# Optimization experiments

Measured on AMD Instinct MI355X. Metric: run time of the kernel, lower is better.

## Reference

```python
import jax, jax.numpy as jnp
import numpy as np
from jax import lax

K = 8  # number of KNN neighbors (excluding self)


def setup_inputs() -> dict:
    key = jax.random.key(0)
    k1, k2, k3 = jax.random.split(key, 3)
    B, H, W, C = 32, 14, 14, 2048
    OUT = 512
    x = jax.random.normal(k1, (B, H, W, C), dtype=jnp.float32)
    W1 = jax.random.normal(k2, (C, OUT), dtype=jnp.float32) * (1.0 / np.sqrt(C))
    b1 = jnp.zeros((OUT,), dtype=jnp.float32)
    W2 = jax.random.normal(k3, (OUT, OUT), dtype=jnp.float32) * (1.0 / np.sqrt(OUT))
    b2 = jnp.zeros((OUT,), dtype=jnp.float32)
    return {"x": x, "W1": W1, "b1": b1, "W2": W2, "b2": b2}


def _knn_edges(xf, k):
    # full pairwise squared-euclidean distance (monotone in cdist p=2)
    sq = jnp.sum(xf * xf, axis=-1)                      # [N]
    d2 = sq[:, None] + sq[None, :] - 2.0 * (xf @ xf.T)  # [N, N]
    _, idx = lax.top_k(-d2, k + 1)                      # smallest k+1
    knn = idx[:, 1:]                                    # drop self
    N = xf.shape[0]
    src = jnp.repeat(jnp.arange(N), k)
    dst = knn.reshape(-1)
    # GCNConv adds self-loops
    loops = jnp.arange(N)
    src = jnp.concatenate([src, loops])
    dst = jnp.concatenate([dst, loops])
    return src, dst


def _gcn_conv(h, W, b, src, dst, N):
    # PyG GCNConv: sym-normalized aggregation with self-loops
    deg = jax.ops.segment_sum(jnp.ones_like(dst, dtype=h.dtype), dst, num_segments=N)
    dinv = lax.rsqrt(jnp.maximum(deg, 1.0))
    norm = dinv[src] * dinv[dst]                        # [E]
    hw = h @ W                                          # [N, F]
    msg = hw[src] * norm[:, None]                       # gather + scale
    out = jax.ops.segment_sum(msg, dst, num_segments=N) # scatter-add
    return out + b


def reference(x, W1, b1, W2, b2):
    B, H, Wd, C = x.shape
    N = B * H * Wd
    xf = x.reshape(N, C)
    src, dst = _knn_edges(xf, K)
    h = jax.nn.relu(_gcn_conv(xf, W1, b1, src, dst, N))
    # dropout is identity in eval mode
    h = jax.nn.relu(_gcn_conv(h, W2, b2, src, dst, N))
    return h.reshape(B, H, Wd, W2.shape[1])
```

## Files before the change

kernel.cpp:

```cpp
#include <hip/hip_runtime.h>

typedef __attribute__((ext_vector_type(8))) _Float16 half8;
typedef __attribute__((ext_vector_type(4))) _Float16 half4;
typedef __attribute__((ext_vector_type(4))) float f32x4;

#define N_NODES 6272
#define CDIM    2048
#define ODIM    512
#define NPAN    49
#define NSLOT   392
#define GRID_G  1232
#define GATE    0.6f

#define XHI_OFF    0ul
#define CANDV_OFF  25690112ul
#define CANDI_OFF  35524608ul
#define SQ_OFF     40441856ul
#define KNN_OFF    40466944ul
#define C16_OFF    40667648ul
#define V16_OFF    41069056ul
#define DEG_OFF    41470464ul
#define CNT_OFF    41495552ul
#define DINV_OFF   41520640ul
#define RPTR_OFF   41545728ul
#define COL_OFF    41571072ul
#define W1T_OFF    41796864ul
#define W2T_OFF    43894016ul
#define HW_OFF     CANDV_OFF
#define H1H_OFF    44418304ul

__device__ __forceinline__ void gld_lds16(const void* g, void* l) {
    __builtin_amdgcn_global_load_lds(
        (const __attribute__((address_space(1))) void*)g,
        (__attribute__((address_space(3))) void*)l, 16, 0, 0);
}

__device__ __forceinline__ half8 frag_read(const char* base, int row, int s, int lane) {
    int b = (s * 4 + (lane >> 4)) ^ (row & 7);
    return *(const half8*)(base + row * 128 + b * 16);
}

#define MF(a, b, c) __builtin_amdgcn_mfma_f32_16x16x32_f16(a, b, c, 0, 0, 0)

__global__ __launch_bounds__(64) void conv_sq_kernel(const float* __restrict__ x,
        _Float16* __restrict__ xhi, float* __restrict__ sq) {
    int i = blockIdx.x;
    int t = threadIdx.x;
    const float* row = x + (size_t)i * CDIM;
    _Float16* hrow = xhi + (size_t)i * CDIM;
    float s = 0.f;
#pragma unroll
    for (int k = 0; k < 8; k++) {
        float4 v = *(const float4*)(row + (k * 64 + t) * 4);
        half4 h;
        h[0] = (_Float16)v.x; h[1] = (_Float16)v.y;
        h[2] = (_Float16)v.z; h[3] = (_Float16)v.w;
        *(half4*)(hrow + (k * 64 + t) * 4) = h;
        s += v.x * v.x + v.y * v.y + v.z * v.z + v.w * v.w;
    }
#pragma unroll
    for (int off = 32; off; off >>= 1) s += __shfl_down(s, off, 64);
    if (t == 0) sq[i] = s;
}

__global__ __launch_bounds__(256) void wtrans_kernel(const float* __restrict__ W,
        _Float16* __restrict__ Wt, int K, int N) {
    __shared__ float tile[64][65];
    int kb = blockIdx.x * 64, nb = blockIdx.y * 64;
    int tid = threadIdx.x;
    int r = tid >> 2, c0 = (tid & 3) * 16;
#pragma unroll
    for (int u = 0; u < 4; u++) {
        float4 v = *(const float4*)(W + (size_t)(kb + r) * N + nb + c0 + u * 4);
        tile[r][c0 + u * 4 + 0] = v.x; tile[r][c0 + u * 4 + 1] = v.y;
        tile[r][c0 + u * 4 + 2] = v.z; tile[r][c0 + u * 4 + 3] = v.w;
    }
    __syncthreads();
    int rn = tid >> 2, ck0 = (tid & 3) * 16;
#pragma unroll
    for (int u = 0; u < 4; u++) {
        half4 o;
#pragma unroll
        for (int j = 0; j < 4; j++) o[j] = (_Float16)tile[ck0 + u * 4 + j][rn];
        *(half4*)(Wt + (size_t)(nb + rn) * K + kb + ck0 + u * 4) = o;
    }
}

__global__ __launch_bounds__(256, 4) void gram_screen(
        const _Float16* __restrict__ xhi, const float* __restrict__ sq,
        float* __restrict__ candv, unsigned short* __restrict__ candi) {
    __shared__ char lds[32768];
    float* S = (float*)lds;
    float* topv = (float*)(lds + 16896);
    unsigned short* topi = (unsigned short*)(lds + 21504);
#define TOPV(r, k) topv[(r) * 9 + (k)]
#define TOPI(r, k) topi[(r) * 10 + (k)]

    int tid = threadIdx.x, lane = tid & 63, wave = tid >> 6;
    int wr = wave >> 1, wc = wave & 1;
    int l15 = lane & 15, kg = lane >> 4;

    int xcd = blockIdx.x & 7, loc = blockIdx.x >> 3;
    if (xcd != 0 && loc >= 153) return;
    int raster = (xcd == 0) ? loc : (154 + (xcd - 1) * 153 + loc);
    int t = (int)((sqrtf(8.f * (float)raster + 1.f) - 1.f) * 0.5f);
    while ((t + 1) * (t + 2) / 2 <= raster) t++;
    while (t * (t + 1) / 2 > raster) t--;
    int p = raster - t * (t + 1) / 2;
    size_t i0 = (size_t)p * 128, j0 = (size_t)t * 128;

    f32x4 acc[4][4] = {};

    int r_in = lane >> 3;
    int skb = (lane & 7) ^ r_in;

#pragma unroll 1
    for (int c = 0; c < 32; c++) {
        int kk = c * 64;
#pragma unroll
        for (int g = 0; g < 8; g++) {
            int sg = wave * 8 + g;
            int tI = sg >> 4, seg = sg & 15;
            size_t row = (tI ? j0 : i0) + (size_t)(seg * 8 + r_in);
            gld_lds16(xhi + row * CDIM + kk + skb * 8, lds + tI * 16384 + seg * 1024);
        }
        __syncthreads();
#pragma unroll
        for (int s = 0; s < 2; s++) {
            half8 a4[4];
#pragma unroll
            for (int m = 0; m < 4; m++)
                a4[m] = frag_read(lds, wr * 64 + m * 16 + l15, s, lane);
#pragma unroll
            for (int n = 0; n < 4; n++) {
                half8 b = frag_read(lds + 16384, wc * 64 + n * 16 + l15, s, lane);
#pragma unroll
                for (int m = 0; m < 4; m++) acc[m][n] = MF(a4[m], b, acc[m][n]);
            }
        }
        __syncthreads();
    }

    float sqi[4][4];
#pragma unroll
    for (int m = 0; m < 4; m++)
#pragma unroll
        for (int r = 0; r < 4; r++)
            sqi[m][r] = sq[(int)i0 + wr * 64 + m * 16 + kg * 4 + r];
    float sqj[4];
#pragma unroll
    for (int n = 0; n < 4; n++)
        sqj[n] = sq[(int)j0 + wc * 64 + n * 16 + l15];

    if (tid < 128) {
#pragma unroll
        for (int k = 0; k < 8; k++) { TOPV(tid, k) = 3.4e38f; TOPI(tid, k) = 0xFFFF; }
    }

#pragma unroll
    for (int cs = 0; cs < 4; cs++) {
        __syncthreads();
        if (wc == (cs >> 1)) {
            const int n0 = (cs & 1) * 2;
#pragma unroll
            for (int m = 0; m < 4; m++)
#pragma unroll
                for (int nn = 0; nn < 2; nn++)
#pragma unroll
                    for (int r = 0; r < 4; r++) {
                        int row = wr * 64 + m * 16 + kg * 4 + r;
                        float d2 = sqi[m][r] + sqj[n0 + nn] - 2.f * acc[m][n0 + nn][r];
                        S[row * 33 + nn * 16 + l15] = d2;
                    }
        }
        __syncthreads();
        if (tid < 128) {
            int r = tid, gi = (int)i0 + r;
            int cbase = (int)j0 + cs * 32;
#pragma unroll 4
            for (int jj = 0; jj < 32; jj++) {
                int gj = cbase + jj;
                if (gj == gi) continue;
                float v = S[r * 33 + jj];
                float wv = TOPV(r, 7); int wi = TOPI(r, 7);
                if (v < wv || (v == wv && gj < wi)) {
                    int pos = 7;
                    while (pos > 0) {
                        float pv = TOPV(r, pos - 1); int pi = TOPI(r, pos - 1);
                        if (v < pv || (v == pv && gj < pi)) {
                            TOPV(r, pos) = pv; TOPI(r, pos) = (unsigned short)pi; pos--;
                        } else break;
                    }
                    TOPV(r, pos) = v; TOPI(r, pos) = (unsigned short)gj;
                }
            }
        }
    }
    __syncthreads();
    if (tid < 128) {
        int gi = (int)i0 + tid;
#pragma unroll
        for (int k = 0; k < 8; k++) {
            candv[(size_t)gi * NSLOT + t * 8 + k] = TOPV(tid, k);
            candi[(size_t)gi * NSLOT + t * 8 + k] = TOPI(tid, k);
        }
#pragma unroll
        for (int k = 0; k < 8; k++) { TOPV(tid, k) = 3.4e38f; TOPI(tid, k) = 0xFFFF; }
    }

    if (p < t) {
#pragma unroll
        for (int ss = 0; ss < 4; ss++) {
            __syncthreads();
            if (wr == (ss >> 1)) {
                const int mb = (ss & 1) * 2;
#pragma unroll
                for (int mm = 0; mm < 2; mm++)
#pragma unroll
                    for (int n = 0; n < 4; n++)
#pragma unroll
                        for (int r = 0; r < 4; r++) {
                            int rl  = mm * 16 + kg * 4 + r;
                            int col = wc * 64 + n * 16 + l15;
                            float d2 = sqi[mb + mm][r] + sqj[n] - 2.f * acc[mb + mm][n][r];
                            S[col * 33 + rl] = d2;
                        }
            }
            __syncthreads();
            if (tid < 128) {
                int cc = tid;
                int rbase = (int)i0 + ss * 32;
#pragma unroll 4
                for (int jj = 0; jj < 32; jj++) {
                    int gi = rbase + jj;
                    float v = S[cc * 33 + jj];
                    float wv = TOPV(cc, 7); int wi = TOPI(cc, 7);
                    if (v < wv || (v == wv && gi < wi)) {
                        int pos = 7;
                        while (pos > 0) {
                            float pv = TOPV(cc, pos - 1); int pi = TOPI(cc, pos - 1);
                            if (v < pv || (v == pv && gi < pi)) {
                                TOPV(cc, pos) = pv; TOPI(cc, pos) = (unsigned short)pi; pos--;
                            } else break;
                        }
                        TOPV(cc, pos) = v; TOPI(cc, pos) = (unsigned short)gi;
                    }
                }
            }
        }
        __syncthreads();
        if (tid < 128) {
            int gj = (int)j0 + tid;
#pragma unroll
            for (int k = 0; k < 8; k++) {
                candv[(size_t)gj * NSLOT + p * 8 + k] = TOPV(tid, k);
                candi[(size_t)gj * NSLOT + p * 8 + k] = TOPI(tid, k);
            }
        }
    }
#undef TOPV
#undef TOPI
}

__global__ __launch_bounds__(256) void merge_topk16_kernel(
        const float* __restrict__ candv, const unsigned short* __restrict__ candi,
        int* __restrict__ cand16, float* __restrict__ val16) {
    int node = blockIdx.x * 4 + (threadIdx.x >> 6);
    int lane = threadIdx.x & 63;
    const float* cv = candv + (size_t)node * NSLOT;
    const unsigned short* ci = candi + (size_t)node * NSLOT;
    float v[7]; int ix[7];
#pragma unroll
    for (int u = 0; u < 7; u++) {
        int s = u * 64 + lane;
        bool ok = (s < NSLOT);
        v[u]  = ok ? cv[s] : 3.4e38f;
        ix[u] = ok ? (int)ci[s] : 0x7fffffff;
    }
#pragma unroll 1
    for (int k = 0; k < 16; k++) {
        float bv = v[0]; int bi = ix[0];
#pragma unroll
        for (int u = 1; u < 7; u++)
            if (v[u] < bv || (v[u] == bv && ix[u] < bi)) { bv = v[u]; bi = ix[u]; }
#pragma unroll
        for (int off = 32; off; off >>= 1) {
            float ov = __shfl_xor(bv, off, 64);
            int   oi = __shfl_xor(bi, off, 64);
            if (ov < bv || (ov == bv && oi < bi)) { bv = ov; bi = oi; }
        }
        if (lane == 0) { cand16[node * 16 + k] = bi; val16[node * 16 + k] = bv; }
#pragma unroll
        for (int u = 0; u < 7; u++)
            if (ix[u] == bi) { v[u] = 3.4e38f; ix[u] = 0x7fffffff; }
    }
}

__global__ __launch_bounds__(256) void refine_kernel(
        const float* __restrict__ x, const float* __restrict__ sq,
        const int* __restrict__ cand16, const float* __restrict__ val16,
        int* __restrict__ knn) {
    int node = blockIdx.x * 4 + (threadIdx.x >> 6);
    int lane = threadIdx.x & 63;
    const int* ci = cand16 + node * 16;
    const float* vi = val16 + node * 16;
    if (vi[8] - vi[7] > GATE) {
        if (lane < 8) knn[(size_t)node * 8 + lane] = ci[lane];
        return;
    }
    const float* xi = x + (size_t)node * CDIM;
    float4 a[8];
#pragma unroll
    for (int g = 0; g < 8; g++) a[g] = *(const float4*)(xi + (g * 64 + lane) * 4);
    float sqi = sq[node];
    float myv = 3.4e38f; int myi = 0x7fffffff;
#pragma unroll 1
    for (int c = 0; c < 16; c++) {
        int j = ci[c];
        const float* xj = x + (size_t)j * CDIM;
        float s = 0.f;
#pragma unroll
        for (int g = 0; g < 8; g++) {
            float4 b = *(const float4*)(xj + (g * 64 + lane) * 4);
            s = fmaf(a[g].x, b.x, s); s = fmaf(a[g].y, b.y, s);
            s = fmaf(a[g].z, b.z, s); s = fmaf(a[g].w, b.w, s);
        }
#pragma unroll
        for (int off = 32; off; off >>= 1) s += __shfl_down(s, off, 64);
        float d2 = sqi + sq[j] - 2.f * s;
        d2 = __shfl(d2, 0, 64);
        if (lane == c) { myv = d2; myi = j; }
    }
#pragma unroll 1
    for (int k = 0; k < 8; k++) {
        float bv = myv; int bi = myi;
#pragma unroll
        for (int off = 8; off; off >>= 1) {
            float ov = __shfl_xor(bv, off, 64);
            int   oi = __shfl_xor(bi, off, 64);
            if (ov < bv || (ov == bv && oi < bi)) { bv = ov; bi = oi; }
        }
        bv = __shfl(bv, lane & 15, 64); bi = __shfl(bi, lane & 15, 64);
        if (lane == 0) knn[(size_t)node * 8 + k] = bi;
        if (myi == bi) { myv = 3.4e38f; myi = 0x7fffffff; }
    }
}

__global__ __launch_bounds__(256) void graph_init_kernel(int* deg, int* cnt) {
    int i = blockIdx.x * 256 + threadIdx.x;
    if (i < N_NODES) { deg[i] = 1; cnt[i] = 0; }
}
__global__ __launch_bounds__(256) void deg_count_kernel(const int* __restrict__ knn,
                                                        int* deg) {
    int e = blockIdx.x * 256 + threadIdx.x;
    if (e < N_NODES * 8) atomicAdd(&deg[knn[e]], 1);
}
__global__ __launch_bounds__(256) void dinv_kernel(const int* __restrict__ deg,
                                                   float* __restrict__ dinv) {
    int i = blockIdx.x * 256 + threadIdx.x;
    if (i < N_NODES) dinv[i] = rsqrtf((float)deg[i]);
}
__global__ __launch_bounds__(256) void scan_kernel(const int* __restrict__ deg,
                                                   int* __restrict__ row_ptr) {
    __shared__ int partial[256];
    const int CHUNK = (N_NODES + 255) / 256;
    int tid = threadIdx.x;
    int start = tid * CHUNK;
    int end = start + CHUNK; if (end > N_NODES) end = N_NODES;
    int s = 0;
    for (int i = start; i < end; i++) s += deg[i];
    partial[tid] = s;
    __syncthreads();
    if (tid == 0) {
        int run = 0;
        for (int k = 0; k < 256; k++) { int v = partial[k]; partial[k] = run; run += v; }
        row_ptr[N_NODES] = run;
    }
    __syncthreads();
    int run = partial[tid];
    for (int i = start; i < end; i++) { row_ptr[i] = run; run += deg[i]; }
}
__global__ __launch_bounds__(256) void scatter_kernel(const int* __restrict__ knn,
        const int* __restrict__ row_ptr, int* cnt, int* __restrict__ col) {
    int i = blockIdx.x * 256 + threadIdx.x;
    if (i >= N_NODES) return;
    int ptr = row_ptr[i] + atomicAdd(&cnt[i], 1);
    col[ptr] = i;
#pragma unroll
    for (int j = 0; j < 8; j++) {
        int d = knn[(size_t)i * 8 + j];
        int q = row_ptr[d] + atomicAdd(&cnt[d], 1);
        col[q] = i;
    }
}

__global__ __launch_bounds__(256) void hgemm_nt_kernel(
        const _Float16* __restrict__ A, const _Float16* __restrict__ Bt,
        float* __restrict__ C, int M, int N, int K) {
    __shared__ char Alds[16384], Blds[16384];
    int tid = threadIdx.x, lane = tid & 63, wave = tid >> 6;
    int wr = wave >> 1, wc = wave & 1;
    int l15 = lane & 15, kg = lane >> 4;
    int nt = N >> 7;
    int i0 = (blockIdx.x / nt) * 128, j0 = (blockIdx.x % nt) * 128;
    f32x4 acc[4][4] = {};

#pragma unroll 1
    for (int kk = 0; kk < K; kk += 64) {
        __syncthreads();
#pragma unroll
        for (int g = 0; g < 4; g++) {
            int R = wave * 32 + g * 8;
            int swzk = ((lane & 7) ^ (lane >> 3)) << 3;
            const _Float16* ga = A + (size_t)(i0 + R + (lane >> 3)) * K + kk + swzk;
            gld_lds16(ga, Alds + R * 128);
            const _Float16* gb = Bt + (size_t)(j0 + R + (lane >> 3)) * K + kk + swzk;
            gld_lds16(gb, Blds + R * 128);
        }
        __syncthreads();
#pragma unroll
        for (int s = 0; s < 2; s++) {
            half8 a[4], b[4];
#pragma unroll
            for (int m = 0; m < 4; m++) a[m] = frag_read(Alds, wr * 64 + m * 16 + l15, s, lane);
#pragma unroll
            for (int n = 0; n < 4; n++) b[n] = frag_read(Blds, wc * 64 + n * 16 + l15, s, lane);
#pragma unroll
            for (int m = 0; m < 4; m++)
#pragma unroll
                for (int n = 0; n < 4; n++)
                    acc[m][n] = __builtin_amdgcn_mfma_f32_16x16x32_f16(a[m], b[n], acc[m][n], 0, 0, 0);
        }
    }
#pragma unroll
    for (int m = 0; m < 4; m++)
#pragma unroll
        for (int n = 0; n < 4; n++)
#pragma unroll
            for (int r = 0; r < 4; r++) {
                int row = i0 + wr * 64 + m * 16 + kg * 4 + r;
                int colj = j0 + wc * 64 + n * 16 + l15;
                C[(size_t)row * N + colj] = acc[m][n][r];
            }
}

template <bool HALF>
__global__ __launch_bounds__(256) void aggregate_kernel(
        const float* __restrict__ hw, const int* __restrict__ row_ptr,
        const int* __restrict__ col, const float* __restrict__ dinv,
        const float* __restrict__ bias, void* __restrict__ outp) {
    int node = blockIdx.x * 4 + (threadIdx.x >> 6);
    int lane = threadIdx.x & 63;
    int e0 = row_ptr[node], e1 = row_ptr[node + 1];
    float4 acc0 = {0.f, 0.f, 0.f, 0.f}, acc1 = {0.f, 0.f, 0.f, 0.f};
    for (int e = e0; e < e1; e++) {
        int s = col[e];
        float w = dinv[s];
        const float* hr = hw + (size_t)s * ODIM;
        float4 v0 = *(const float4*)(hr + lane * 4);
        float4 v1 = *(const float4*)(hr + 256 + lane * 4);
        acc0.x = fmaf(w, v0.x, acc0.x); acc0.y = fmaf(w, v0.y, acc0.y);
        acc0.z = fmaf(w, v0.z, acc0.z); acc0.w = fmaf(w, v0.w, acc0.w);
        acc1.x = fmaf(w, v1.x, acc1.x); acc1.y = fmaf(w, v1.y, acc1.y);
        acc1.z = fmaf(w, v1.z, acc1.z); acc1.w = fmaf(w, v1.w, acc1.w);
    }
    float wd = dinv[node];
    float4 b0 = *(const float4*)(bias + lane * 4);
    float4 b1 = *(const float4*)(bias + 256 + lane * 4);
    float o[8];
    o[0] = fmaxf(fmaf(acc0.x, wd, b0.x), 0.f);
    o[1] = fmaxf(fmaf(acc0.y, wd, b0.y), 0.f);
    o[2] = fmaxf(fmaf(acc0.z, wd, b0.z), 0.f);
    o[3] = fmaxf(fmaf(acc0.w, wd, b0.w), 0.f);
    o[4] = fmaxf(fmaf(acc1.x, wd, b1.x), 0.f);
    o[5] = fmaxf(fmaf(acc1.y, wd, b1.y), 0.f);
    o[6] = fmaxf(fmaf(acc1.z, wd, b1.z), 0.f);
    o[7] = fmaxf(fmaf(acc1.w, wd, b1.w), 0.f);
    if (HALF) {
        _Float16* out = (_Float16*)outp;
        half4 h0, h1;
#pragma unroll
        for (int j = 0; j < 4; j++) { h0[j] = (_Float16)o[j]; h1[j] = (_Float16)o[4 + j]; }
        *(half4*)(out + (size_t)node * ODIM + lane * 4)       = h0;
        *(half4*)(out + (size_t)node * ODIM + 256 + lane * 4) = h1;
    } else {
        float* out = (float*)outp;
        float4 f0 = {o[0], o[1], o[2], o[3]}, f1 = {o[4], o[5], o[6], o[7]};
        *(float4*)(out + (size_t)node * ODIM + lane * 4)       = f0;
        *(float4*)(out + (size_t)node * ODIM + 256 + lane * 4) = f1;
    }
}

extern "C" void kernel_launch(void* const* d_in, const int* in_sizes, int n_in,
                              void* d_out, int out_size, void* d_ws, size_t ws_size,
                              hipStream_t stream) {
    const float* x  = (const float*)d_in[0];
    const float* W1 = (const float*)d_in[1];
    const float* b1 = (const float*)d_in[2];
    const float* W2 = (const float*)d_in[3];
    const float* b2 = (const float*)d_in[4];
    float* out = (float*)d_out;
    char* ws = (char*)d_ws;

    _Float16* xhi  = (_Float16*)(ws + XHI_OFF);
    float* candv   = (float*)(ws + CANDV_OFF);
    unsigned short* candi = (unsigned short*)(ws + CANDI_OFF);
    float* sq      = (float*)(ws + SQ_OFF);
    int*   knn     = (int*)  (ws + KNN_OFF);
    int*   cand16  = (int*)  (ws + C16_OFF);
    float* val16   = (float*)(ws + V16_OFF);
    int*   deg     = (int*)  (ws + DEG_OFF);
    int*   cnt     = (int*)  (ws + CNT_OFF);
    float* dinv    = (float*)(ws + DINV_OFF);
    int*   row_ptr = (int*)  (ws + RPTR_OFF);
    int*   col     = (int*)  (ws + COL_OFF);
    _Float16* w1t  = (_Float16*)(ws + W1T_OFF);
    _Float16* w2t  = (_Float16*)(ws + W2T_OFF);
    float* hw      = (float*)(ws + HW_OFF);
    _Float16* h1h  = (_Float16*)(ws + H1H_OFF);

    conv_sq_kernel<<<N_NODES, 64, 0, stream>>>(x, xhi, sq);
    wtrans_kernel<<<dim3(CDIM / 64, ODIM / 64), 256, 0, stream>>>(W1, w1t, CDIM, ODIM);
    wtrans_kernel<<<dim3(ODIM / 64, ODIM / 64), 256, 0, stream>>>(W2, w2t, ODIM, ODIM);

    gram_screen<<<GRID_G, 256, 0, stream>>>(xhi, sq, candv, candi);
    merge_topk16_kernel<<<N_NODES / 4, 256, 0, stream>>>(candv, candi, cand16, val16);
    refine_kernel<<<N_NODES / 4, 256, 0, stream>>>(x, sq, cand16, val16, knn);

    graph_init_kernel<<<(N_NODES + 255) / 256, 256, 0, stream>>>(deg, cnt);
    deg_count_kernel<<<(N_NODES * 8) / 256, 256, 0, stream>>>(knn, deg);
    dinv_kernel<<<(N_NODES + 255) / 256, 256, 0, stream>>>(deg, dinv);
    scan_kernel<<<1, 256, 0, stream>>>(deg, row_ptr);
    scatter_kernel<<<(N_NODES + 255) / 256, 256, 0, stream>>>(knn, row_ptr, cnt, col);

    hgemm_nt_kernel<<<(N_NODES / 128) * (ODIM / 128), 256, 0, stream>>>(xhi, w1t, hw, N_NODES, ODIM, CDIM);
    aggregate_kernel<true><<<N_NODES / 4, 256, 0, stream>>>(hw, row_ptr, col, dinv, b1, (void*)h1h);
    hgemm_nt_kernel<<<(N_NODES / 128) * (ODIM / 128), 256, 0, stream>>>(h1h, w2t, hw, N_NODES, ODIM, ODIM);
    aggregate_kernel<false><<<N_NODES / 4, 256, 0, stream>>>(hw, row_ptr, col, dinv, b2, (void*)out);
}
```

Baseline: 1.197 ms.

## Fuse prep, KNN select/refine, and graph-build kernels; change gram K-chunk addressing

Merges the fp16 conversion and squared-norm pass with both weight transposes into one prep launch. Fuses the top-16 merge with the exact-distance refine, passing candidates through lane registers and shuffles instead of global memory. Replaces the five graph-construction kernels (init, degree count, dinv, scan, scatter) with a single 1024-thread block that does all of it with LDS atomics. It also changes which K columns the Gram screen loads per chunk: each step now fetches two 32-wide slices from the two halves of the row. Together these aim to cut launch overhead and global round trips, but the graph build now runs serially on one workgroup.

```diff
diff --git a/kernel.cpp b/kernel.cpp
--- a/kernel.cpp
+++ b/kernel.cpp
@@ -17,10 +17,7 @@
 #define CANDI_OFF  35524608ul
 #define SQ_OFF     40441856ul
 #define KNN_OFF    40466944ul
-#define C16_OFF    40667648ul
-#define V16_OFF    41069056ul
 #define DEG_OFF    41470464ul
-#define CNT_OFF    41495552ul
 #define DINV_OFF   41520640ul
 #define RPTR_OFF   41545728ul
 #define COL_OFF    41571072ul
@@ -42,32 +39,37 @@
 
 #define MF(a, b, c) __builtin_amdgcn_mfma_f32_16x16x32_f16(a, b, c, 0, 0, 0)
 
-__global__ __launch_bounds__(64) void conv_sq_kernel(const float* __restrict__ x,
-        _Float16* __restrict__ xhi, float* __restrict__ sq) {
-    int i = blockIdx.x;
-    int t = threadIdx.x;
-    const float* row = x + (size_t)i * CDIM;
-    _Float16* hrow = xhi + (size_t)i * CDIM;
-    float s = 0.f;
-#pragma unroll
-    for (int k = 0; k < 8; k++) {
-        float4 v = *(const float4*)(row + (k * 64 + t) * 4);
-        half4 h;
-        h[0] = (_Float16)v.x; h[1] = (_Float16)v.y;
-        h[2] = (_Float16)v.z; h[3] = (_Float16)v.w;
-        *(half4*)(hrow + (k * 64 + t) * 4) = h;
-        s += v.x * v.x + v.y * v.y + v.z * v.z + v.w * v.w;
-    }
-#pragma unroll
-    for (int off = 32; off; off >>= 1) s += __shfl_down(s, off, 64);
-    if (t == 0) sq[i] = s;
-}
-
-__global__ __launch_bounds__(256) void wtrans_kernel(const float* __restrict__ W,
-        _Float16* __restrict__ Wt, int K, int N) {
+__global__ __launch_bounds__(256) void prep_kernel(const float* __restrict__ x,
+        _Float16* __restrict__ xhi, float* __restrict__ sq,
+        const float* __restrict__ W1, _Float16* __restrict__ w1t,
+        const float* __restrict__ W2, _Float16* __restrict__ w2t) {
     __shared__ float tile[64][65];
-    int kb = blockIdx.x * 64, nb = blockIdx.y * 64;
-    int tid = threadIdx.x;
+    int bid = blockIdx.x, tid = threadIdx.x;
+    if (bid < 1568) {
+        int i = bid * 4 + (tid >> 6);
+        int t = tid & 63;
+        const float* row = x + (size_t)i * CDIM;
+        _Float16* hrow = xhi + (size_t)i * CDIM;
+        float s = 0.f;
+#pragma unroll
+        for (int k = 0; k < 8; k++) {
+            float4 v = *(const float4*)(row + (k * 64 + t) * 4);
+            half4 h;
+            h[0] = (_Float16)v.x; h[1] = (_Float16)v.y;
+            h[2] = (_Float16)v.z; h[3] = (_Float16)v.w;
+            *(half4*)(hrow + (k * 64 + t) * 4) = h;
+            s += v.x * v.x + v.y * v.y + v.z * v.z + v.w * v.w;
+        }
+#pragma unroll
+        for (int off = 32; off; off >>= 1) s += __shfl_down(s, off, 64);
+        if (t == 0) sq[i] = s;
+        return;
+    }
+    const float* W; _Float16* Wt; int K, N, idx;
+    if (bid < 1824) { idx = bid - 1568; W = W1; Wt = w1t; K = CDIM; N = ODIM; }
+    else            { idx = bid - 1824; W = W2; Wt = w2t; K = ODIM; N = ODIM; }
+    int nkb = K / 64;
+    int kb = (idx % nkb) * 64, nb = (idx / nkb) * 64;
     int r = tid >> 2, c0 = (tid & 3) * 16;
 #pragma unroll
     for (int u = 0; u < 4; u++) {
@@ -112,17 +114,18 @@
     f32x4 acc[4][4] = {};
 
     int r_in = lane >> 3;
-    int skb = (lane & 7) ^ r_in;
+    int kb = (lane & 7) ^ r_in;
+    int kadd = (kb < 4) ? kb * 8 : 1024 + (kb - 4) * 8;
 
 #pragma unroll 1
     for (int c = 0; c < 32; c++) {
-        int kk = c * 64;
+        int kk = c * 32;
 #pragma unroll
         for (int g = 0; g < 8; g++) {
             int sg = wave * 8 + g;
             int tI = sg >> 4, seg = sg & 15;
             size_t row = (tI ? j0 : i0) + (size_t)(seg * 8 + r_in);
-            gld_lds16(xhi + row * CDIM + kk + skb * 8, lds + tI * 16384 + seg * 1024);
+            gld_lds16(xhi + row * CDIM + kk + kadd, lds + tI * 16384 + seg * 1024);
         }
         __syncthreads();
 #pragma unroll
@@ -262,9 +265,10 @@
 #undef TOPI
 }
 
-__global__ __launch_bounds__(256) void merge_topk16_kernel(
+__global__ __launch_bounds__(256) void knn_select_kernel(
         const float* __restrict__ candv, const unsigned short* __restrict__ candi,
-        int* __restrict__ cand16, float* __restrict__ val16) {
+        const float* __restrict__ x, const float* __restrict__ sq,
+        int* __restrict__ knn) {
     int node = blockIdx.x * 4 + (threadIdx.x >> 6);
     int lane = threadIdx.x & 63;
     const float* cv = candv + (size_t)node * NSLOT;
@@ -277,6 +281,7 @@
         v[u]  = ok ? cv[s] : 3.4e38f;
         ix[u] = ok ? (int)ci[s] : 0x7fffffff;
     }
+    float myv16 = 3.4e38f; int myc = 0x7fffffff;
 #pragma unroll 1
     for (int k = 0; k < 16; k++) {
         float bv = v[0]; int bi = ix[0];
@@ -289,23 +294,14 @@
             int   oi = __shfl_xor(bi, off, 64);
             if (ov < bv || (ov == bv && oi < bi)) { bv = ov; bi = oi; }
         }
-        if (lane == 0) { cand16[node * 16 + k] = bi; val16[node * 16 + k] = bv; }
+        if (lane == k) { myv16 = bv; myc = bi; }
 #pragma unroll
         for (int u = 0; u < 7; u++)
             if (ix[u] == bi) { v[u] = 3.4e38f; ix[u] = 0x7fffffff; }
     }
-}
-
-__global__ __launch_bounds__(256) void refine_kernel(
-        const float* __restrict__ x, const float* __restrict__ sq,
-        const int* __restrict__ cand16, const float* __restrict__ val16,
-        int* __restrict__ knn) {
-    int node = blockIdx.x * 4 + (threadIdx.x >> 6);
-    int lane = threadIdx.x & 63;
-    const int* ci = cand16 + node * 16;
-    const float* vi = val16 + node * 16;
-    if (vi[8] - vi[7] > GATE) {
-        if (lane < 8) knn[(size_t)node * 8 + lane] = ci[lane];
+    float g7 = __shfl(myv16, 7, 64), g8 = __shfl(myv16, 8, 64);
+    if (g8 - g7 > GATE) {
+        if (lane < 8) knn[(size_t)node * 8 + lane] = myc;
         return;
     }
     const float* xi = x + (size_t)node * CDIM;
@@ -313,10 +309,10 @@
 #pragma unroll
     for (int g = 0; g < 8; g++) a[g] = *(const float4*)(xi + (g * 64 + lane) * 4);
     float sqi = sq[node];
-    float myv = 3.4e38f; int myi = 0x7fffffff;
+    float rv = 3.4e38f; int ri = 0x7fffffff;
 #pragma unroll 1
     for (int c = 0; c < 16; c++) {
-        int j = ci[c];
+        int j = __shfl(myc, c, 64);
         const float* xj = x + (size_t)j * CDIM;
         float s = 0.f;
 #pragma unroll
@@ -329,11 +325,11 @@
         for (int off = 32; off; off >>= 1) s += __shfl_down(s, off, 64);
         float d2 = sqi + sq[j] - 2.f * s;
         d2 = __shfl(d2, 0, 64);
-        if (lane == c) { myv = d2; myi = j; }
+        if (lane == c) { rv = d2; ri = j; }
     }
 #pragma unroll 1
     for (int k = 0; k < 8; k++) {
-        float bv = myv; int bi = myi;
+        float bv = rv; int bi = ri;
 #pragma unroll
         for (int off = 8; off; off >>= 1) {
             float ov = __shfl_xor(bv, off, 64);
@@ -342,55 +338,51 @@
         }
         bv = __shfl(bv, lane & 15, 64); bi = __shfl(bi, lane & 15, 64);
         if (lane == 0) knn[(size_t)node * 8 + k] = bi;
-        if (myi == bi) { myv = 3.4e38f; myi = 0x7fffffff; }
-    }
-}
-
-__global__ __launch_bounds__(256) void graph_init_kernel(int* deg, int* cnt) {
-    int i = blockIdx.x * 256 + threadIdx.x;
-    if (i < N_NODES) { deg[i] = 1; cnt[i] = 0; }
-}
-__global__ __launch_bounds__(256) void deg_count_kernel(const int* __restrict__ knn,
-                                                        int* deg) {
-    int e = blockIdx.x * 256 + threadIdx.x;
-    if (e < N_NODES * 8) atomicAdd(&deg[knn[e]], 1);
-}
-__global__ __launch_bounds__(256) void dinv_kernel(const int* __restrict__ deg,
-                                                   float* __restrict__ dinv) {
-    int i = blockIdx.x * 256 + threadIdx.x;
-    if (i < N_NODES) dinv[i] = rsqrtf((float)deg[i]);
-}
-__global__ __launch_bounds__(256) void scan_kernel(const int* __restrict__ deg,
-                                                   int* __restrict__ row_ptr) {
-    __shared__ int partial[256];
-    const int CHUNK = (N_NODES + 255) / 256;
+        if (ri == bi) { rv = 3.4e38f; ri = 0x7fffffff; }
+    }
+}
+
+__global__ __launch_bounds__(1024) void graph_build_kernel(
+        const int* __restrict__ knn, float* __restrict__ dinv,
+        int* __restrict__ row_ptr, int* __restrict__ col) {
+    __shared__ int deg_l[N_NODES];
+    __shared__ int cnt_l[N_NODES];
+    __shared__ int rp_l[N_NODES];
+    __shared__ int partial[1024];
     int tid = threadIdx.x;
-    int start = tid * CHUNK;
-    int end = start + CHUNK; if (end > N_NODES) end = N_NODES;
+    for (int i = tid; i < N_NODES; i += 1024) { deg_l[i] = 1; cnt_l[i] = 0; }
+    __syncthreads();
+    for (int e = tid; e < N_NODES * 8; e += 1024) atomicAdd(&deg_l[knn[e]], 1);
+    __syncthreads();
+    const int CH = 7;
+    int start = tid * CH;
+    int end = start + CH; if (end > N_NODES) end = N_NODES;
     int s = 0;
-    for (int i = start; i < end; i++) s += deg[i];
+    for (int i = start; i < end; i++) s += deg_l[i];
     partial[tid] = s;
     __syncthreads();
     if (tid == 0) {
         int run = 0;
-        for (int k = 0; k < 256; k++) { int v = partial[k]; partial[k] = run; run += v; }
+        for (int k = 0; k < 1024; k++) { int vv = partial[k]; partial[k] = run; run += vv; }
         row_ptr[N_NODES] = run;
     }
     __syncthreads();
     int run = partial[tid];
-    for (int i = start; i < end; i++) { row_ptr[i] = run; run += deg[i]; }
-}
-__global__ __launch_bounds__(256) void scatter_kernel(const int* __restrict__ knn,
-        const int* __restrict__ row_ptr, int* cnt, int* __restrict__ col) {
-    int i = blockIdx.x * 256 + threadIdx.x;
-    if (i >= N_NODES) return;
-    int ptr = row_ptr[i] + atomicAdd(&cnt[i], 1);
-    col[ptr] = i;
-#pragma unroll
-    for (int j = 0; j < 8; j++) {
-        int d = knn[(size_t)i * 8 + j];
-        int q = row_ptr[d] + atomicAdd(&cnt[d], 1);
-        col[q] = i;
+    for (int i = start; i < end; i++) {
+        rp_l[i] = run; row_ptr[i] = run;
+        dinv[i] = rsqrtf((float)deg_l[i]);
+        run += deg_l[i];
+    }
+    __syncthreads();
+    for (int i = tid; i < N_NODES; i += 1024) {
+        int p0 = rp_l[i] + atomicAdd(&cnt_l[i], 1);
+        col[p0] = i;
+#pragma unroll
+        for (int j = 0; j < 8; j++) {
+            int d = knn[i * 8 + j];
+            int q = rp_l[d] + atomicAdd(&cnt_l[d], 1);
+            col[q] = i;
+        }
     }
 }
 
@@ -507,10 +499,6 @@
     unsigned short* candi = (unsigned short*)(ws + CANDI_OFF);
     float* sq      = (float*)(ws + SQ_OFF);
     int*   knn     = (int*)  (ws + KNN_OFF);
-    int*   cand16  = (int*)  (ws + C16_OFF);
-    float* val16   = (float*)(ws + V16_OFF);
-    int*   deg     = (int*)  (ws + DEG_OFF);
-    int*   cnt     = (int*)  (ws + CNT_OFF);
     float* dinv    = (float*)(ws + DINV_OFF);
     int*   row_ptr = (int*)  (ws + RPTR_OFF);
     int*   col     = (int*)  (ws + COL_OFF);
@@ -519,19 +507,10 @@
     float* hw      = (float*)(ws + HW_OFF);
     _Float16* h1h  = (_Float16*)(ws + H1H_OFF);
 
-    conv_sq_kernel<<<N_NODES, 64, 0, stream>>>(x, xhi, sq);
-    wtrans_kernel<<<dim3(CDIM / 64, ODIM / 64), 256, 0, stream>>>(W1, w1t, CDIM, ODIM);
-    wtrans_kernel<<<dim3(ODIM / 64, ODIM / 64), 256, 0, stream>>>(W2, w2t, ODIM, ODIM);
-
+    prep_kernel<<<1888, 256, 0, stream>>>(x, xhi, sq, W1, w1t, W2, w2t);
     gram_screen<<<GRID_G, 256, 0, stream>>>(xhi, sq, candv, candi);
-    merge_topk16_kernel<<<N_NODES / 4, 256, 0, stream>>>(candv, candi, cand16, val16);
-    refine_kernel<<<N_NODES / 4, 256, 0, stream>>>(x, sq, cand16, val16, knn);
-
-    graph_init_kernel<<<(N_NODES + 255) / 256, 256, 0, stream>>>(deg, cnt);
-    deg_count_kernel<<<(N_NODES * 8) / 256, 256, 0, stream>>>(knn, deg);
-    dinv_kernel<<<(N_NODES + 255) / 256, 256, 0, stream>>>(deg, dinv);
-    scan_kernel<<<1, 256, 0, stream>>>(deg, row_ptr);
-    scatter_kernel<<<(N_NODES + 255) / 256, 256, 0, stream>>>(knn, row_ptr, cnt, col);
+    knn_select_kernel<<<N_NODES / 4, 256, 0, stream>>>(candv, candi, x, sq, knn);
+    graph_build_kernel<<<1, 1024, 0, stream>>>(knn, dinv, row_ptr, col);
 
     hgemm_nt_kernel<<<(N_NODES / 128) * (ODIM / 128), 256, 0, stream>>>(xhi, w1t, hw, N_NODES, ODIM, CDIM);
     aggregate_kernel<true><<<N_NODES / 4, 256, 0, stream>>>(hw, row_ptr, col, dinv, b1, (void*)h1h);
```

Measured after the change: 1.181 ms. Within noise of the previous version (-1.4%).
